# Kernel tuning notes

Hardware: AMD Instinct MI355X
Metric: run time of the kernel (lower is better)

Reference implementation:

```python
import jax, jax.numpy as jnp
import numpy as np

B, S, D_MODEL, N_HEADS = 2, 2048, 1024, 16
HEAD_DIM = D_MODEL // N_HEADS  # 64
SCALE = HEAD_DIM ** -0.5
MASK_FILL = -1e9


def setup_inputs() -> dict:
    key = jax.random.key(0)
    k1, k2, k3 = jax.random.split(key, 3)
    x = jax.random.normal(k1, (B, S, D_MODEL), dtype=jnp.float32)
    # nn.Linear weight [3*d_att, d_model], trunc_normal std=0.02 style init
    W_qkv = jax.random.normal(k2, (3 * D_MODEL, D_MODEL), dtype=jnp.float32) * 0.02
    # boolean attention mask over the full [b, s_q, h, t_k] score tensor (True = keep)
    mask = jax.random.bernoulli(k3, p=0.9, shape=(B, S, N_HEADS, S))
    return {"x": x, "W_qkv": W_qkv, "mask": mask}


def reference(x, W_qkv, mask):
    b, s, dm = x.shape
    h, d = N_HEADS, HEAD_DIM
    # fused QKV projection (no bias): [b,s,3*dm] -> [b,s,3,h,d]
    qkv = jnp.einsum('bsm,nm->bsn', x, W_qkv).reshape(b, s, 3, h, d)
    q, k, v = qkv[:, :, 0], qkv[:, :, 1], qkv[:, :, 2]
    # scores: [b, s_q, h, t_k]
    attn = jnp.einsum('bshd,bthd->bsht', q, k) * SCALE
    attn = jnp.where(mask, attn, MASK_FILL)
    attn = jax.nn.softmax(attn, axis=-1)
    # out[b,t,h,d] = sum_s attn[b,t,h,s] * v[b,s,h,d]  (original einsum 'b s h d, b t h s -> b t h d')
    out = jnp.einsum('bshd,bths->bthd', v, attn)
    return out.reshape(b, s, h * d)  # proj is Identity (d_out=None)
```

## Files before the change

kernel.cpp:

```cpp
#include <hip/hip_runtime.h>

#define S_   2048
#define DM_  1024
#define NH_  16
#define HD_  64
#define KDIM 1024

typedef __attribute__((ext_vector_type(8))) short  shortx8;
typedef __attribute__((ext_vector_type(4))) float  floatx4;

#define AS1 __attribute__((address_space(1)))
#define AS3 __attribute__((address_space(3)))

__device__ __forceinline__ unsigned short f2bf(float f) {
  unsigned u = __float_as_uint(f);
  u += 0x7FFFu + ((u >> 16) & 1u);
  return (unsigned short)(u >> 16);
}

__device__ __forceinline__ void gld_lds16(const void* g, unsigned short* l) {
  __builtin_amdgcn_global_load_lds((const AS1 void*)g, (AS3 void*)l, 16, 0, 0);
}

__global__ __launch_bounds__(256) void detect_kernel(const unsigned* __restrict__ mask,
                                                     const unsigned* __restrict__ x,
                                                     int* __restrict__ flags)
{
  __shared__ int s[5];
  if (threadIdx.x == 0) { s[0]=1; s[1]=1; s[2]=1; s[3]=1; s[4]=0; }
  __syncthreads();
  bool o32=true, of32=true, o16=true, o8=true;
  for (int i = threadIdx.x; i < 16384; i += 256) {
    unsigned v = mask[i];
    o32 &= (v <= 1u);
    of32 &= (v == 0u) || (v == 0x3F800000u);
    unsigned lo = v & 0xFFFFu, hi = v >> 16;
    o16 &= ((lo==0u)||(lo==0x3F80u)) && ((hi==0u)||(hi==0x3F80u));
    o8  &= ((v & 0xFEFEFEFEu) == 0u);
  }
  int cnt = 0;
  for (int i = threadIdx.x; i < 4096; i += 256) {
    unsigned v = x[i];
    unsigned b1 = (v >> 8) & 0x7Fu;
    cnt += (b1 >= 0x32u && b1 <= 0x41u) ? 1 : 0;
  }
  if (!o32)  atomicAnd(&s[0], 0);
  if (!of32) atomicAnd(&s[1], 0);
  if (!o16)  atomicAnd(&s[2], 0);
  if (!o8)   atomicAnd(&s[3], 0);
  atomicAdd(&s[4], cnt);
  __syncthreads();
  if (threadIdx.x == 0) {
    int mf;
    if (s[0]) mf = 0; else if (s[1]) mf = 3; else if (s[2]) mf = 2; else mf = 1;
    flags[0] = mf;
    flags[1] = (s[4] > 2048) ? 1 : 0;
  }
}

__global__ __launch_bounds__(256) void qkv_gemm(const void* __restrict__ Xv,
                                                const void* __restrict__ Wv,
                                                unsigned short* __restrict__ Qg,
                                                unsigned short* __restrict__ Kg,
                                                unsigned short* __restrict__ Vt,
                                                const int* __restrict__ flags)
{
  __shared__ unsigned short lA[128*64];
  __shared__ unsigned short lB[128*64];
  const int tid  = threadIdx.x;
  const int wid  = tid >> 6,  lane = tid & 63;
  const int quad = lane >> 4, l16  = lane & 15;
  const int bm = blockIdx.x, bn = blockIdx.y;
  const int wM = (wid >> 1) * 64, wN = (wid & 1) * 64;
  const int xbf = flags[1];

  floatx4 acc[4][4] = {};

  for (int kt = 0; kt < KDIM; kt += 64) {
    __syncthreads();
    if (xbf) {
      const unsigned short* X = (const unsigned short*)Xv;
      const unsigned short* W = (const unsigned short*)Wv;
      #pragma unroll
      for (int p = 0; p < 4; ++p) {
        int chunk = p*256 + tid;
        int r = chunk >> 3, c = chunk & 7;
        gld_lds16(X + (size_t)(bm*128 + r)*KDIM + kt + c*8, lA + chunk*8);
      }
      #pragma unroll
      for (int p = 0; p < 4; ++p) {
        int chunk = p*256 + tid;
        int r = chunk >> 3, c = chunk & 7;
        gld_lds16(W + (size_t)(bn*128 + r)*KDIM + kt + c*8, lB + chunk*8);
      }
    } else {
      const float* X = (const float*)Xv;
      const float* W = (const float*)Wv;
      #pragma unroll
      for (int p = 0; p < 8; ++p) {
        int c4 = p*256 + tid;
        int r = c4 >> 4, c = c4 & 15;
        float4 v = *(const float4*)(X + (size_t)(bm*128 + r)*KDIM + kt + c*4);
        unsigned short* d = lA + r*64 + c*4;
        d[0]=f2bf(v.x); d[1]=f2bf(v.y); d[2]=f2bf(v.z); d[3]=f2bf(v.w);
      }
      #pragma unroll
      for (int p = 0; p < 8; ++p) {
        int c4 = p*256 + tid;
        int r = c4 >> 4, c = c4 & 15;
        float4 v = *(const float4*)(W + (size_t)(bn*128 + r)*KDIM + kt + c*4);
        unsigned short* d = lB + r*64 + c*4;
        d[0]=f2bf(v.x); d[1]=f2bf(v.y); d[2]=f2bf(v.z); d[3]=f2bf(v.w);
      }
    }
    __syncthreads();

    #pragma unroll
    for (int ks = 0; ks < 2; ++ks) {
      shortx8 af[4], bfr[4];
      #pragma unroll
      for (int mi = 0; mi < 4; ++mi)
        af[mi] = *(const shortx8*)(lA + (wM + mi*16 + l16)*64 + ks*32 + quad*8);
      #pragma unroll
      for (int ni = 0; ni < 4; ++ni)
        bfr[ni] = *(const shortx8*)(lB + (wN + ni*16 + l16)*64 + ks*32 + quad*8);
      #pragma unroll
      for (int mi = 0; mi < 4; ++mi)
        #pragma unroll
        for (int ni = 0; ni < 4; ++ni)
          acc[mi][ni] = __builtin_amdgcn_mfma_f32_16x16x32_bf16(af[mi], bfr[ni], acc[mi][ni], 0, 0, 0);
    }
  }

  if (bn < 8) {
    #pragma unroll
    for (int mi = 0; mi < 4; ++mi)
      #pragma unroll
      for (int ni = 0; ni < 4; ++ni)
        #pragma unroll
        for (int r = 0; r < 4; ++r) {
          int m = bm*128 + wM + mi*16 + quad*4 + r;
          int n = bn*128 + wN + ni*16 + l16;
          int b = m >> 11, q = m & 2047, h = n >> 6, d = n & 63;
          Qg[(((size_t)(b*NH_ + h))*S_ + q)*HD_ + d] = f2bf(acc[mi][ni][r] * 0.125f);
        }
  } else if (bn < 16) {
    #pragma unroll
    for (int mi = 0; mi < 4; ++mi)
      #pragma unroll
      for (int ni = 0; ni < 4; ++ni)
        #pragma unroll
        for (int r = 0; r < 4; ++r) {
          int m = bm*128 + wM + mi*16 + quad*4 + r;
          int n = bn*128 + wN + ni*16 + l16 - 1024;
          int b = m >> 11, t = m & 2047, h = n >> 6, d = n & 63;
          Kg[(((size_t)(b*NH_ + h))*S_ + t)*HD_ + d] = f2bf(acc[mi][ni][r]);
        }
  } else {
    #pragma unroll
    for (int mi = 0; mi < 4; ++mi)
      #pragma unroll
      for (int ni = 0; ni < 4; ++ni) {
        int m0 = bm*128 + wM + mi*16 + quad*4;
        int n  = bn*128 + wN + ni*16 + l16 - 2048;
        int b = m0 >> 11, t = m0 & 2047, h = n >> 6, d = n & 63;
        ushort4 u;
        u.x = f2bf(acc[mi][ni][0]); u.y = f2bf(acc[mi][ni][1]);
        u.z = f2bf(acc[mi][ni][2]); u.w = f2bf(acc[mi][ni][3]);
        *(ushort4*)(Vt + (((size_t)(b*NH_ + h))*HD_ + d)*S_ + t) = u;
      }
  }
}

__global__ __launch_bounds__(256, 4) void attn_kernel(const unsigned short* __restrict__ Qg,
                                                      const unsigned short* __restrict__ Kg,
                                                      const unsigned short* __restrict__ Vt,
                                                      const void* __restrict__ maskp,
                                                      const int* __restrict__ flags,
                                                      void* __restrict__ outv)
{
  __shared__ unsigned short lK[2][64*64];
  __shared__ unsigned short lVt[2][64*64];
  __shared__ unsigned short lQP[4][16*64];

  const int tid  = threadIdx.x;
  const int wid  = tid >> 6,  lane = tid & 63;
  const int quad = lane >> 4, l16  = lane & 15;
  const int qb = blockIdx.x * 64;
  const int h  = blockIdx.y, b = blockIdx.z;
  const int bh = b*NH_ + h;
  const int mflag = flags[0];
  const int obf   = flags[1];

  #pragma unroll
  for (int p = 0; p < 2; ++p) {
    int chunk = p*256 + tid;
    gld_lds16(Qg + ((size_t)bh*S_ + qb)*HD_ + chunk*8, (unsigned short*)lQP + chunk*8);
  }

  auto stage = [&](int t0, int buf) {
    #pragma unroll
    for (int p = 0; p < 2; ++p) {
      int chunk = p*256 + tid;
      gld_lds16(Kg + ((size_t)bh*S_ + t0)*HD_ + chunk*8, lK[buf] + chunk*8);
    }
    #pragma unroll
    for (int p = 0; p < 2; ++p) {
      int chunk = p*256 + tid;
      int r = chunk >> 3, c = chunk & 7;
      gld_lds16(Vt + ((size_t)bh*HD_ + r)*S_ + t0 + c*8, lVt[buf] + chunk*8);
    }
  };

  size_t mrow[4];
  #pragma unroll
  for (int r = 0; r < 4; ++r) {
    int q = qb + wid*16 + quad*4 + r;
    mrow[r] = (((size_t)b*S_ + q)*NH_ + h)*S_ + l16;
  }

  auto loadmask = [&](int t0, unsigned (*mz)[4]) {
    if (mflag == 1) {
      const unsigned char* mp = (const unsigned char*)maskp;
      #pragma unroll
      for (int tile = 0; tile < 4; ++tile)
        #pragma unroll
        for (int r = 0; r < 4; ++r) mz[tile][r] = mp[mrow[r] + t0 + tile*16];
    } else if (mflag == 2) {
      const unsigned short* mp = (const unsigned short*)maskp;
      #pragma unroll
      for (int tile = 0; tile < 4; ++tile)
        #pragma unroll
        for (int r = 0; r < 4; ++r) mz[tile][r] = mp[mrow[r] + t0 + tile*16];
    } else {
      const unsigned* mp = (const unsigned*)maskp;
      #pragma unroll
      for (int tile = 0; tile < 4; ++tile)
        #pragma unroll
        for (int r = 0; r < 4; ++r) mz[tile][r] = mp[mrow[r] + t0 + tile*16];
    }
  };

  unsigned mc[4][4], mn[4][4];
  stage(0, 0);
  loadmask(0, mc);
  __syncthreads();

  shortx8 qf[2];
  #pragma unroll
  for (int ks = 0; ks < 2; ++ks)
    qf[ks] = *(const shortx8*)((const unsigned short*)lQP + (wid*16 + l16)*64 + ks*32 + quad*8);

  floatx4 acc[4] = {};
  float lsum[4] = {0.f, 0.f, 0.f, 0.f};
  unsigned short* lPw = lQP[wid];

  for (int t0 = 0; t0 < S_; t0 += 64) {
    const int cur = (t0 >> 6) & 1;
    if (t0 + 64 < S_) {
      stage(t0 + 64, cur ^ 1);
      loadmask(t0 + 64, mn);
    }

    floatx4 sc[4] = {};
    #pragma unroll
    for (int tile = 0; tile < 4; ++tile)
      #pragma unroll
      for (int ks = 0; ks < 2; ++ks) {
        shortx8 kf = *(const shortx8*)(lK[cur] + (tile*16 + l16)*64 + ks*32 + quad*8);
        sc[tile] = __builtin_amdgcn_mfma_f32_16x16x32_bf16(qf[ks], kf, sc[tile], 0, 0, 0);
      }

    #pragma unroll
    for (int tile = 0; tile < 4; ++tile)
      #pragma unroll
      for (int r = 0; r < 4; ++r) {
        float e = __expf(sc[tile][r]);
        e = mc[tile][r] ? e : 0.f;
        lsum[r] += e;
        int row = quad*4 + r;
        int col = tile*16 + l16;
        lPw[(row << 6) + (((col >> 3) ^ (row & 7)) << 3) + (col & 7)] = f2bf(e);
      }

    #pragma unroll
    for (int ks = 0; ks < 2; ++ks) {
      shortx8 pa = *(const shortx8*)(lPw + (l16 << 6) + ((((ks*4 + quad)) ^ (l16 & 7)) << 3));
      #pragma unroll
      for (int d = 0; d < 4; ++d) {
        shortx8 vb = *(const shortx8*)(lVt[cur] + (d*16 + l16)*64 + ks*32 + quad*8);
        acc[d] = __builtin_amdgcn_mfma_f32_16x16x32_bf16(pa, vb, acc[d], 0, 0, 0);
      }
    }

    #pragma unroll
    for (int tile = 0; tile < 4; ++tile)
      #pragma unroll
      for (int r = 0; r < 4; ++r) mc[tile][r] = mn[tile][r];

    __syncthreads();
  }

  float rinv[4];
  #pragma unroll
  for (int r = 0; r < 4; ++r) {
    float l = lsum[r];
    #pragma unroll
    for (int o = 1; o < 16; o <<= 1) l += __shfl_xor(l, o);
    rinv[r] = 1.f / l;
  }

  #pragma unroll
  for (int d = 0; d < 4; ++d)
    #pragma unroll
    for (int r = 0; r < 4; ++r) {
      int q = qb + wid*16 + quad*4 + r;
      size_t oi = ((size_t)b*S_ + q)*DM_ + h*HD_ + d*16 + l16;
      float v = acc[d][r] * rinv[r];
      if (obf) ((unsigned short*)outv)[oi] = f2bf(v);
      else     ((float*)outv)[oi]          = v;
    }
}

extern "C" void kernel_launch(void* const* d_in, const int* in_sizes, int n_in,
                              void* d_out, int out_size, void* d_ws, size_t ws_size,
                              hipStream_t stream) {
  (void)in_sizes; (void)n_in; (void)out_size; (void)ws_size;
  const void* X    = d_in[0];
  const void* W    = d_in[1];
  const void* mask = d_in[2];
  int* flags = (int*)d_ws;
  const size_t SEG = (size_t)2*NH_*S_*HD_*2;
  unsigned short* Qg = (unsigned short*)((char*)d_ws + 256);
  unsigned short* Kg = (unsigned short*)((char*)d_ws + 256 + SEG);
  unsigned short* Vt = (unsigned short*)((char*)d_ws + 256 + 2*SEG);

  detect_kernel<<<1, 256, 0, stream>>>((const unsigned*)mask, (const unsigned*)X, flags);
  qkv_gemm<<<dim3(32, 24), 256, 0, stream>>>(X, W, Qg, Kg, Vt, flags);
  attn_kernel<<<dim3(32, 16, 2), 256, 0, stream>>>(Qg, Kg, Vt, mask, flags, d_out);
}
```

Before: 886.4 us.

## Enlarge attention query block, pack mask bits, inline dtype detection

The attention kernel now handles 128 queries per block (32 per wave) instead of 64, so each staged K/V tile is reused across twice as many query rows and the number of K/V loads per output is halved. Mask values are packed into a 32-bit register bitmask instead of 16 separate words, and launch bounds drop to 2 blocks per SM to make room for the extra registers. The separate single-block detect kernel is removed: dtype detection now runs per block from a small sample with ballots, which saves one launch but checks a smaller sample. The risks are lower occupancy, half as many attention blocks in the grid, and less robust format detection.

After: 851.1 us. 1.04x faster.

```diff
diff --git a/kernel.cpp b/kernel.cpp
--- a/kernel.cpp
+++ b/kernel.cpp
@@ -5,6 +5,7 @@
 #define NH_  16
 #define HD_  64
 #define KDIM 1024
+#define QB_  128
 
 typedef __attribute__((ext_vector_type(8))) short  shortx8;
 typedef __attribute__((ext_vector_type(4))) float  floatx4;
@@ -22,57 +23,32 @@
   __builtin_amdgcn_global_load_lds((const AS1 void*)g, (AS3 void*)l, 16, 0, 0);
 }
 
-__global__ __launch_bounds__(256) void detect_kernel(const unsigned* __restrict__ mask,
-                                                     const unsigned* __restrict__ x,
-                                                     int* __restrict__ flags)
-{
-  __shared__ int s[5];
-  if (threadIdx.x == 0) { s[0]=1; s[1]=1; s[2]=1; s[3]=1; s[4]=0; }
-  __syncthreads();
-  bool o32=true, of32=true, o16=true, o8=true;
-  for (int i = threadIdx.x; i < 16384; i += 256) {
-    unsigned v = mask[i];
-    o32 &= (v <= 1u);
-    of32 &= (v == 0u) || (v == 0x3F800000u);
-    unsigned lo = v & 0xFFFFu, hi = v >> 16;
-    o16 &= ((lo==0u)||(lo==0x3F80u)) && ((hi==0u)||(hi==0x3F80u));
-    o8  &= ((v & 0xFEFEFEFEu) == 0u);
-  }
-  int cnt = 0;
-  for (int i = threadIdx.x; i < 4096; i += 256) {
-    unsigned v = x[i];
-    unsigned b1 = (v >> 8) & 0x7Fu;
-    cnt += (b1 >= 0x32u && b1 <= 0x41u) ? 1 : 0;
-  }
-  if (!o32)  atomicAnd(&s[0], 0);
-  if (!of32) atomicAnd(&s[1], 0);
-  if (!o16)  atomicAnd(&s[2], 0);
-  if (!o8)   atomicAnd(&s[3], 0);
-  atomicAdd(&s[4], cnt);
-  __syncthreads();
-  if (threadIdx.x == 0) {
-    int mf;
-    if (s[0]) mf = 0; else if (s[1]) mf = 3; else if (s[2]) mf = 2; else mf = 1;
-    flags[0] = mf;
-    flags[1] = (s[4] > 2048) ? 1 : 0;
-  }
-}
-
 __global__ __launch_bounds__(256) void qkv_gemm(const void* __restrict__ Xv,
                                                 const void* __restrict__ Wv,
                                                 unsigned short* __restrict__ Qg,
                                                 unsigned short* __restrict__ Kg,
-                                                unsigned short* __restrict__ Vt,
-                                                const int* __restrict__ flags)
+                                                unsigned short* __restrict__ Vt)
 {
   __shared__ unsigned short lA[128*64];
   __shared__ unsigned short lB[128*64];
+  __shared__ int sx;
   const int tid  = threadIdx.x;
   const int wid  = tid >> 6,  lane = tid & 63;
   const int quad = lane >> 4, l16  = lane & 15;
   const int bm = blockIdx.x, bn = blockIdx.y;
   const int wM = (wid >> 1) * 64, wN = (wid & 1) * 64;
-  const int xbf = flags[1];
+
+  if (tid == 0) sx = 0;
+  __syncthreads();
+  {
+    unsigned xv = ((const unsigned*)Xv)[tid];
+    unsigned b1 = (xv >> 8) & 0x7Fu;
+    bool pb = (b1 >= 0x32u && b1 <= 0x41u);
+    unsigned long long bal = __ballot(pb);
+    if (lane == 0) atomicAdd(&sx, (int)__popcll(bal));
+  }
+  __syncthreads();
+  const int xbf = sx > 128;
 
   floatx4 acc[4][4] = {};
 
@@ -172,30 +148,53 @@
   }
 }
 
-__global__ __launch_bounds__(256, 4) void attn_kernel(const unsigned short* __restrict__ Qg,
+__global__ __launch_bounds__(256, 2) void attn_kernel(const unsigned short* __restrict__ Qg,
                                                       const unsigned short* __restrict__ Kg,
                                                       const unsigned short* __restrict__ Vt,
                                                       const void* __restrict__ maskp,
-                                                      const int* __restrict__ flags,
+                                                      const void* __restrict__ xg,
                                                       void* __restrict__ outv)
 {
-  __shared__ unsigned short lK[2][64*64];
-  __shared__ unsigned short lVt[2][64*64];
-  __shared__ unsigned short lQP[4][16*64];
+  __shared__ unsigned short lQ[QB_*HD_];
+  __shared__ unsigned short lK[2][64*HD_];
+  __shared__ unsigned short lVt[2][HD_*64];
+  __shared__ int sdet[5];
 
   const int tid  = threadIdx.x;
   const int wid  = tid >> 6,  lane = tid & 63;
   const int quad = lane >> 4, l16  = lane & 15;
-  const int qb = blockIdx.x * 64;
+  const int qb = blockIdx.x * QB_;
   const int h  = blockIdx.y, b = blockIdx.z;
   const int bh = b*NH_ + h;
-  const int mflag = flags[0];
-  const int obf   = flags[1];
-
-  #pragma unroll
-  for (int p = 0; p < 2; ++p) {
+
+  if (tid < 5) sdet[tid] = (tid == 4) ? 0 : 1;
+  __syncthreads();
+  {
+    unsigned mv = ((const unsigned*)maskp)[tid];
+    bool o32  = (mv <= 1u);
+    bool of32 = (mv == 0u) || (mv == 0x3F800000u);
+    unsigned lo = mv & 0xFFFFu, hi = mv >> 16;
+    bool o16 = ((lo==0u)||(lo==0x3F80u)) && ((hi==0u)||(hi==0x3F80u));
+    bool o8  = ((mv & 0xFEFEFEFEu) == 0u);
+    unsigned xv = ((const unsigned*)xg)[tid];
+    unsigned b1 = (xv >> 8) & 0x7Fu;
+    bool pb = (b1 >= 0x32u && b1 <= 0x41u);
+    unsigned long long B0 = __ballot(o32), B1 = __ballot(of32);
+    unsigned long long B2 = __ballot(o16), B3 = __ballot(o8);
+    unsigned long long BX = __ballot(pb);
+    if (lane == 0) {
+      if (~B0) atomicAnd(&sdet[0], 0);
+      if (~B1) atomicAnd(&sdet[1], 0);
+      if (~B2) atomicAnd(&sdet[2], 0);
+      if (~B3) atomicAnd(&sdet[3], 0);
+      atomicAdd(&sdet[4], (int)__popcll(BX));
+    }
+  }
+
+  #pragma unroll
+  for (int p = 0; p < 4; ++p) {
     int chunk = p*256 + tid;
-    gld_lds16(Qg + ((size_t)bh*S_ + qb)*HD_ + chunk*8, (unsigned short*)lQP + chunk*8);
+    gld_lds16(Qg + ((size_t)bh*S_ + qb)*HD_ + chunk*8, lQ + chunk*8);
   }
 
   auto stage = [&](int t0, int buf) {
@@ -212,114 +211,154 @@
     }
   };
 
-  size_t mrow[4];
-  #pragma unroll
-  for (int r = 0; r < 4; ++r) {
-    int q = qb + wid*16 + quad*4 + r;
-    mrow[r] = (((size_t)b*S_ + q)*NH_ + h)*S_ + l16;
-  }
-
-  auto loadmask = [&](int t0, unsigned (*mz)[4]) {
+  size_t mrow[2][4];
+  #pragma unroll
+  for (int qh = 0; qh < 2; ++qh)
+    #pragma unroll
+    for (int r = 0; r < 4; ++r) {
+      int q = qb + wid*32 + qh*16 + quad*4 + r;
+      mrow[qh][r] = (((size_t)b*S_ + q)*NH_ + h)*S_ + l16;
+    }
+
+  stage(0, 0);
+  __syncthreads();
+
+  const int mflag = sdet[0] ? 0 : (sdet[1] ? 3 : (sdet[2] ? 2 : 1));
+  const int obf   = sdet[4] > 128;
+
+  auto loadraw = [&](int t0, unsigned (*mz)[4][4]) {
     if (mflag == 1) {
       const unsigned char* mp = (const unsigned char*)maskp;
       #pragma unroll
-      for (int tile = 0; tile < 4; ++tile)
-        #pragma unroll
-        for (int r = 0; r < 4; ++r) mz[tile][r] = mp[mrow[r] + t0 + tile*16];
+      for (int qh = 0; qh < 2; ++qh)
+        #pragma unroll
+        for (int r = 0; r < 4; ++r)
+          #pragma unroll
+          for (int tile = 0; tile < 4; ++tile) mz[qh][r][tile] = mp[mrow[qh][r] + t0 + tile*16];
     } else if (mflag == 2) {
       const unsigned short* mp = (const unsigned short*)maskp;
       #pragma unroll
-      for (int tile = 0; tile < 4; ++tile)
-        #pragma unroll
-        for (int r = 0; r < 4; ++r) mz[tile][r] = mp[mrow[r] + t0 + tile*16];
+      for (int qh = 0; qh < 2; ++qh)
+        #pragma unroll
+        for (int r = 0; r < 4; ++r)
+          #pragma unroll
+          for (int tile = 0; tile < 4; ++tile) mz[qh][r][tile] = mp[mrow[qh][r] + t0 + tile*16];
     } else {
       const unsigned* mp = (const unsigned*)maskp;
       #pragma unroll
-      for (int tile = 0; tile < 4; ++tile)
-        #pragma unroll
-        for (int r = 0; r < 4; ++r) mz[tile][r] = mp[mrow[r] + t0 + tile*16];
+      for (int qh = 0; qh < 2; ++qh)
+        #pragma unroll
+        for (int r = 0; r < 4; ++r)
+          #pragma unroll
+          for (int tile = 0; tile < 4; ++tile) mz[qh][r][tile] = mp[mrow[qh][r] + t0 + tile*16];
     }
   };
 
-  unsigned mc[4][4], mn[4][4];
-  stage(0, 0);
-  loadmask(0, mc);
-  __syncthreads();
-
-  shortx8 qf[2];
-  #pragma unroll
-  for (int ks = 0; ks < 2; ++ks)
-    qf[ks] = *(const shortx8*)((const unsigned short*)lQP + (wid*16 + l16)*64 + ks*32 + quad*8);
-
-  floatx4 acc[4] = {};
-  float lsum[4] = {0.f, 0.f, 0.f, 0.f};
-  unsigned short* lPw = lQP[wid];
+  shortx8 qf[2][2];
+  #pragma unroll
+  for (int qh = 0; qh < 2; ++qh)
+    #pragma unroll
+    for (int ks = 0; ks < 2; ++ks)
+      qf[qh][ks] = *(const shortx8*)(lQ + (wid*32 + qh*16 + l16)*HD_ + ks*32 + quad*8);
+
+  floatx4 acc[2][4] = {};
+  float lsum[2][4] = {};
+  unsigned short* lPw = lQ + wid*2048;
+
+  unsigned mc = 0;
+  {
+    unsigned m0[2][4][4];
+    loadraw(0, m0);
+    #pragma unroll
+    for (int qh = 0; qh < 2; ++qh)
+      #pragma unroll
+      for (int r = 0; r < 4; ++r)
+        #pragma unroll
+        for (int tile = 0; tile < 4; ++tile)
+          mc |= (m0[qh][r][tile] != 0u ? 1u : 0u) << (qh*16 + r*4 + tile);
+  }
 
   for (int t0 = 0; t0 < S_; t0 += 64) {
     const int cur = (t0 >> 6) & 1;
-    if (t0 + 64 < S_) {
+    unsigned mraw[2][4][4];
+    const bool more = (t0 + 64 < S_);
+    if (more) {
       stage(t0 + 64, cur ^ 1);
-      loadmask(t0 + 64, mn);
-    }
-
-    floatx4 sc[4] = {};
-    #pragma unroll
-    for (int tile = 0; tile < 4; ++tile)
+      loadraw(t0 + 64, mraw);
+    }
+
+    #pragma unroll
+    for (int qh = 0; qh < 2; ++qh) {
+      floatx4 sc[4] = {};
+      #pragma unroll
+      for (int tile = 0; tile < 4; ++tile)
+        #pragma unroll
+        for (int ks = 0; ks < 2; ++ks) {
+          shortx8 kf = *(const shortx8*)(lK[cur] + (tile*16 + l16)*64 + ks*32 + quad*8);
+          sc[tile] = __builtin_amdgcn_mfma_f32_16x16x32_bf16(qf[qh][ks], kf, sc[tile], 0, 0, 0);
+        }
+
+      #pragma unroll
+      for (int tile = 0; tile < 4; ++tile)
+        #pragma unroll
+        for (int r = 0; r < 4; ++r) {
+          float e = __expf(sc[tile][r]);
+          e = (mc & (1u << (qh*16 + r*4 + tile))) ? e : 0.f;
+          lsum[qh][r] += e;
+          int row = qh*16 + quad*4 + r;
+          int col = tile*16 + l16;
+          lPw[(row << 6) + (((col >> 3) ^ (row & 7)) << 3) + (col & 7)] = f2bf(e);
+        }
+
       #pragma unroll
       for (int ks = 0; ks < 2; ++ks) {
-        shortx8 kf = *(const shortx8*)(lK[cur] + (tile*16 + l16)*64 + ks*32 + quad*8);
-        sc[tile] = __builtin_amdgcn_mfma_f32_16x16x32_bf16(qf[ks], kf, sc[tile], 0, 0, 0);
-      }
-
-    #pragma unroll
-    for (int tile = 0; tile < 4; ++tile)
+        int prow = qh*16 + l16;
+        shortx8 pa = *(const shortx8*)(lPw + (prow << 6) + (((ks*4 + quad) ^ (prow & 7)) << 3));
+        #pragma unroll
+        for (int d = 0; d < 4; ++d) {
+          shortx8 vb = *(const shortx8*)(lVt[cur] + (d*16 + l16)*64 + ks*32 + quad*8);
+          acc[qh][d] = __builtin_amdgcn_mfma_f32_16x16x32_bf16(pa, vb, acc[qh][d], 0, 0, 0);
+        }
+      }
+    }
+
+    unsigned mcn = 0;
+    if (more) {
+      #pragma unroll
+      for (int qh = 0; qh < 2; ++qh)
+        #pragma unroll
+        for (int r = 0; r < 4; ++r)
+          #pragma unroll
+          for (int tile = 0; tile < 4; ++tile)
+            mcn |= (mraw[qh][r][tile] != 0u ? 1u : 0u) << (qh*16 + r*4 + tile);
+    }
+    __syncthreads();
+    mc = mcn;
+  }
+
+  float rinv[2][4];
+  #pragma unroll
+  for (int qh = 0; qh < 2; ++qh)
+    #pragma unroll
+    for (int r = 0; r < 4; ++r) {
+      float l = lsum[qh][r];
+      #pragma unroll
+      for (int o = 1; o < 16; o <<= 1) l += __shfl_xor(l, o);
+      rinv[qh][r] = 1.f / l;
+    }
+
+  #pragma unroll
+  for (int qh = 0; qh < 2; ++qh)
+    #pragma unroll
+    for (int d = 0; d < 4; ++d)
       #pragma unroll
       for (int r = 0; r < 4; ++r) {
-        float e = __expf(sc[tile][r]);
-        e = mc[tile][r] ? e : 0.f;
-        lsum[r] += e;
-        int row = quad*4 + r;
-        int col = tile*16 + l16;
-        lPw[(row << 6) + (((col >> 3) ^ (row & 7)) << 3) + (col & 7)] = f2bf(e);
-      }
-
-    #pragma unroll
-    for (int ks = 0; ks < 2; ++ks) {
-      shortx8 pa = *(const shortx8*)(lPw + (l16 << 6) + ((((ks*4 + quad)) ^ (l16 & 7)) << 3));
-      #pragma unroll
-      for (int d = 0; d < 4; ++d) {
-        shortx8 vb = *(const shortx8*)(lVt[cur] + (d*16 + l16)*64 + ks*32 + quad*8);
-        acc[d] = __builtin_amdgcn_mfma_f32_16x16x32_bf16(pa, vb, acc[d], 0, 0, 0);
-      }
-    }
-
-    #pragma unroll
-    for (int tile = 0; tile < 4; ++tile)
-      #pragma unroll
-      for (int r = 0; r < 4; ++r) mc[tile][r] = mn[tile][r];
-
-    __syncthreads();
-  }
-
-  float rinv[4];
-  #pragma unroll
-  for (int r = 0; r < 4; ++r) {
-    float l = lsum[r];
-    #pragma unroll
-    for (int o = 1; o < 16; o <<= 1) l += __shfl_xor(l, o);
-    rinv[r] = 1.f / l;
-  }
-
-  #pragma unroll
-  for (int d = 0; d < 4; ++d)
-    #pragma unroll
-    for (int r = 0; r < 4; ++r) {
-      int q = qb + wid*16 + quad*4 + r;
-      size_t oi = ((size_t)b*S_ + q)*DM_ + h*HD_ + d*16 + l16;
-      float v = acc[d][r] * rinv[r];
-      if (obf) ((unsigned short*)outv)[oi] = f2bf(v);
-      else     ((float*)outv)[oi]          = v;
-    }
+        int q = qb + wid*32 + qh*16 + quad*4 + r;
+        size_t oi = ((size_t)b*S_ + q)*DM_ + h*HD_ + d*16 + l16;
+        float v = acc[qh][d][r] * rinv[qh][r];
+        if (obf) ((unsigned short*)outv)[oi] = f2bf(v);
+        else     ((float*)outv)[oi]          = v;
+      }
 }
 
 extern "C" void kernel_launch(void* const* d_in, const int* in_sizes, int n_in,
@@ -329,13 +368,11 @@
   const void* X    = d_in[0];
   const void* W    = d_in[1];
   const void* mask = d_in[2];
-  int* flags = (int*)d_ws;
   const size_t SEG = (size_t)2*NH_*S_*HD_*2;
   unsigned short* Qg = (unsigned short*)((char*)d_ws + 256);
   unsigned short* Kg = (unsigned short*)((char*)d_ws + 256 + SEG);
   unsigned short* Vt = (unsigned short*)((char*)d_ws + 256 + 2*SEG);
 
-  detect_kernel<<<1, 256, 0, stream>>>((const unsigned*)mask, (const unsigned*)X, flags);
-  qkv_gemm<<<dim3(32, 24), 256, 0, stream>>>(X, W, Qg, Kg, Vt, flags);
-  attn_kernel<<<dim3(32, 16, 2), 256, 0, stream>>>(Qg, Kg, Vt, mask, flags, d_out);
-}
+  qkv_gemm<<<dim3(32, 24), 256, 0, stream>>>(X, W, Qg, Kg, Vt);
+  attn_kernel<<<dim3(S_/QB_, NH_, 2), 256, 0, stream>>>(Qg, Kg, Vt, mask, X, d_out);
+}
```
